# Kernel optimization log

Hardware: AMD Instinct MI355X
Metric: run time of the kernel (lower is better)

Reference implementation:

```python
import jax, jax.numpy as jnp
import numpy as np

B, T, C, H = 4, 2048, 2048, 16
HD = C // H  # head_size = 128
EPS = 1e-5


def layernorm(x, g, b):
    mu = jnp.mean(x, axis=-1, keepdims=True)
    var = jnp.var(x, axis=-1, keepdims=True)
    return (x - mu) * jax.lax.rsqrt(var + EPS) * g + b


def setup_inputs() -> dict:
    key = jax.random.key(0)
    ks = jax.random.split(key, 12)
    s_attn = 1.0 / np.sqrt(C)
    s_ffn1 = 1.0 / np.sqrt(C)
    s_ffn2 = 1.0 / np.sqrt(4 * C)
    return {
        "x": jax.random.normal(ks[0], (B, T, C), jnp.float32),
        "Wq": jax.random.normal(ks[1], (H, C, HD), jnp.float32) * s_attn,
        "Wk": jax.random.normal(ks[2], (H, C, HD), jnp.float32) * s_attn,
        "Wv": jax.random.normal(ks[3], (H, C, HD), jnp.float32) * s_attn,
        "Wp": jax.random.normal(ks[4], (C, C), jnp.float32) * s_attn,
        "bp": jnp.zeros((C,), jnp.float32),
        "W1": jax.random.normal(ks[5], (C, 4 * C), jnp.float32) * s_ffn1,
        "b1": jnp.zeros((4 * C,), jnp.float32),
        "W2": jax.random.normal(ks[6], (4 * C, C), jnp.float32) * s_ffn2,
        "b2": jnp.zeros((C,), jnp.float32),
        "g1": jnp.ones((C,), jnp.float32),
        "beta1": jnp.zeros((C,), jnp.float32),
        "g2": jnp.ones((C,), jnp.float32),
        "beta2": jnp.zeros((C,), jnp.float32),
    }


def reference(x, Wq, Wk, Wv, Wp, bp, W1, b1, W2, b2, g1, beta1, g2, beta2):
    # --- attention sublayer (pre-LN, causal) ---
    h = layernorm(x, g1, beta1)
    q = jnp.einsum("btc,hcd->bhtd", h, Wq)
    k = jnp.einsum("bsc,hcd->bhsd", h, Wk)
    v = jnp.einsum("bsc,hcd->bhsd", h, Wv)
    scores = jnp.einsum("bhtd,bhsd->bhts", q, k) / jnp.sqrt(jnp.asarray(HD, x.dtype))
    causal = jnp.tril(jnp.ones((T, T), bool))
    scores = jnp.where(causal, scores, jnp.asarray(-jnp.inf, x.dtype))
    w = jax.nn.softmax(scores, axis=-1)  # dropout = identity (eval mode)
    o = jnp.einsum("bhts,bhsd->bhtd", w, v)
    o = o.transpose(0, 2, 1, 3).reshape(B, T, C)  # concat heads
    x = x + o @ Wp + bp
    # --- feed-forward sublayer ---
    h2 = layernorm(x, g2, beta2)
    f = jax.nn.gelu(h2 @ W1 + b1, approximate=False)
    x = x + f @ W2 + b2
    return x
```

## Files before the change

### kernel.cpp

```cpp
#include <hip/hip_runtime.h>
#include <math.h>

#define B_ 4
#define T_ 2048
#define C_ 2048
#define H_ 16
#define HD_ 128

typedef __attribute__((ext_vector_type(8))) short short8;
typedef __attribute__((ext_vector_type(4))) float f32x4;
typedef unsigned short u16;
typedef unsigned int u32;

__device__ __forceinline__ u16 f2bf(float f) {
  union { float f; unsigned u; } v; v.f = f;
  unsigned r = v.u + 0x7FFFu + ((v.u >> 16) & 1u);
  return (u16)(r >> 16);
}

__device__ __forceinline__ void gld16(const void* g, void* l) {
  __builtin_amdgcn_global_load_lds(
      (__attribute__((address_space(1))) void*)(void*)g,
      (__attribute__((address_space(3))) void*)l, 16, 0, 0);
}

__global__ __launch_bounds__(256) void tconv(const float* __restrict__ in,
                                             u16* __restrict__ out,
                                             int K, int N,
                                             long inBS, long outBS) {
  __shared__ float tile[32][33];
  const float* inb = in + (long)blockIdx.z * inBS;
  u16* outb = out + (long)blockIdx.z * outBS;
  int k0 = blockIdx.x << 5, n0 = blockIdx.y << 5;
  int t = threadIdx.x;
  {
    int kk = t >> 3, nn = (t & 7) << 2;
    float4 v = *(const float4*)(inb + (long)(k0 + kk) * N + n0 + nn);
    tile[kk][nn + 0] = v.x; tile[kk][nn + 1] = v.y;
    tile[kk][nn + 2] = v.z; tile[kk][nn + 3] = v.w;
  }
  __syncthreads();
  {
    int nn = t >> 3, kk = (t & 7) << 2;
    ushort4 o;
    o.x = f2bf(tile[kk + 0][nn]); o.y = f2bf(tile[kk + 1][nn]);
    o.z = f2bf(tile[kk + 2][nn]); o.w = f2bf(tile[kk + 3][nn]);
    *(ushort4*)(outb + (long)(n0 + nn) * K + k0 + kk) = o;
  }
}

__global__ __launch_bounds__(256) void ln_rows(const float* __restrict__ x,
                                               const float* __restrict__ gam,
                                               const float* __restrict__ bet,
                                               u16* __restrict__ out) {
  int row = blockIdx.x;
  const float* xr = x + (size_t)row * C_;
  int t = threadIdx.x;
  float4 v0 = *(const float4*)(xr + t * 8);
  float4 v1 = *(const float4*)(xr + t * 8 + 4);
  float s = v0.x + v0.y + v0.z + v0.w + v1.x + v1.y + v1.z + v1.w;
  float ss = v0.x * v0.x + v0.y * v0.y + v0.z * v0.z + v0.w * v0.w +
             v1.x * v1.x + v1.y * v1.y + v1.z * v1.z + v1.w * v1.w;
  for (int d = 32; d > 0; d >>= 1) {
    s += __shfl_down(s, d);
    ss += __shfl_down(ss, d);
  }
  __shared__ float red[8];
  int wv = t >> 6;
  if ((t & 63) == 0) { red[wv] = s; red[4 + wv] = ss; }
  __syncthreads();
  s = red[0] + red[1] + red[2] + red[3];
  ss = red[4] + red[5] + red[6] + red[7];
  float mu = s * (1.0f / C_);
  float var = ss * (1.0f / C_) - mu * mu;
  float rs = rsqrtf(var + 1e-5f);
  int c = t * 8;
  float vv[8] = {v0.x, v0.y, v0.z, v0.w, v1.x, v1.y, v1.z, v1.w};
  ushort4 o0, o1;
  o0.x = f2bf((vv[0] - mu) * rs * gam[c + 0] + bet[c + 0]);
  o0.y = f2bf((vv[1] - mu) * rs * gam[c + 1] + bet[c + 1]);
  o0.z = f2bf((vv[2] - mu) * rs * gam[c + 2] + bet[c + 2]);
  o0.w = f2bf((vv[3] - mu) * rs * gam[c + 3] + bet[c + 3]);
  o1.x = f2bf((vv[4] - mu) * rs * gam[c + 4] + bet[c + 4]);
  o1.y = f2bf((vv[5] - mu) * rs * gam[c + 5] + bet[c + 5]);
  o1.z = f2bf((vv[6] - mu) * rs * gam[c + 6] + bet[c + 6]);
  o1.w = f2bf((vv[7] - mu) * rs * gam[c + 7] + bet[c + 7]);
  *(ushort4*)(out + (size_t)row * C_ + c) = o0;
  *(ushort4*)(out + (size_t)row * C_ + c + 4) = o1;
}

template <int EPI>
__global__ __launch_bounds__(512, 2) void gemm256(
    const u16* __restrict__ A, const u16* __restrict__ BT,
    int M, int N, int K, int lda, int ldb,
    u16* __restrict__ oq, u16* __restrict__ ok, u16* __restrict__ ovt,
    float* __restrict__ of32, const float* __restrict__ resid,
    const float* __restrict__ bias, u16* __restrict__ obf, int addBias) {
  extern __shared__ char smem[];
  int nbx = N >> 8;
  int nwg = gridDim.x;
  int flat = blockIdx.x;
  int sw = (flat & 7) * (nwg >> 3) + (flat >> 3);
  int bx = sw % nbx, by = sw / nbx;
  int m0 = by << 8, n0 = bx << 8;
  int tid = threadIdx.x;
  int lane = tid & 63, wave = tid >> 6;
  int wm = wave >> 2, wn = wave & 3;
  int l15 = lane & 15, l16 = lane >> 4;
  int nt = K >> 6;

  f32x4 acc[8][4] = {};
  short8 afA[4][2], afB[4][2], bfA[2][2], bfB[2][2];

  auto stage = [&](int b, int r, int k0) {
    int row = (r & 3) * 64 + (tid >> 3);
    int lslot = (tid & 7) ^ (row & 7);
    char* dst = smem + ((r < 4) ? 0 : 65536) + b * 32768 + (r & 3) * 8192 + tid * 16;
    const u16* src = ((r < 4) ? (A + (long)(m0 + row) * lda)
                              : (BT + (long)(n0 + row) * ldb)) +
                     k0 + lslot * 8;
    gld16(src, dst);
  };
  auto ldA = [&](int cur, int mf, int kk) {
    int row = wm * 128 + mf * 16 + l15;
    int slot = (kk * 4 + l16) ^ (row & 7);
    return *(const short8*)(smem + cur * 32768 + row * 128 + slot * 16);
  };
  auto ldB = [&](int cur, int nf, int kk) {
    int row = wn * 64 + nf * 16 + l15;
    int slot = (kk * 4 + l16) ^ (row & 7);
    return *(const short8*)(smem + 65536 + cur * 32768 + row * 128 + slot * 16);
  };

#pragma unroll
  for (int r = 0; r < 8; ++r) stage(0, r, 0);
  __syncthreads();

#pragma unroll
  for (int mq = 0; mq < 4; ++mq)
#pragma unroll
    for (int kk = 0; kk < 2; ++kk) afA[mq][kk] = ldA(0, mq, kk);
#pragma unroll
  for (int nq = 0; nq < 2; ++nq)
#pragma unroll
    for (int kk = 0; kk < 2; ++kk) bfA[nq][kk] = ldB(0, nq, kk);

  for (int t = 0; t < nt; ++t) {
    int cur = t & 1, nxt = cur ^ 1;
    bool more = (t + 1) < nt;
    int k1 = (t + 1) << 6;
    if (more) {
#pragma unroll
      for (int r = 0; r < 8; ++r) stage(nxt, r, k1);
    }
#pragma unroll
    for (int nq = 0; nq < 2; ++nq)
#pragma unroll
      for (int kk = 0; kk < 2; ++kk) bfB[nq][kk] = ldB(cur, 2 + nq, kk);
    __builtin_amdgcn_s_setprio(1);
#pragma unroll
    for (int mq = 0; mq < 4; ++mq)
#pragma unroll
      for (int nq = 0; nq < 2; ++nq)
#pragma unroll
        for (int kk = 0; kk < 2; ++kk)
          acc[mq][nq] = __builtin_amdgcn_mfma_f32_16x16x32_bf16(
              afA[mq][kk], bfA[nq][kk], acc[mq][nq], 0, 0, 0);
    __builtin_amdgcn_s_setprio(0);
#pragma unroll
    for (int mq = 0; mq < 4; ++mq)
#pragma unroll
      for (int kk = 0; kk < 2; ++kk) afB[mq][kk] = ldA(cur, 4 + mq, kk);
    __builtin_amdgcn_s_setprio(1);
#pragma unroll
    for (int mq = 0; mq < 4; ++mq)
#pragma unroll
      for (int nq = 0; nq < 2; ++nq)
#pragma unroll
        for (int kk = 0; kk < 2; ++kk)
          acc[mq][2 + nq] = __builtin_amdgcn_mfma_f32_16x16x32_bf16(
              afA[mq][kk], bfB[nq][kk], acc[mq][2 + nq], 0, 0, 0);
    __builtin_amdgcn_s_setprio(0);
    __builtin_amdgcn_s_setprio(1);
#pragma unroll
    for (int mq = 0; mq < 4; ++mq)
#pragma unroll
      for (int nq = 0; nq < 2; ++nq)
#pragma unroll
        for (int kk = 0; kk < 2; ++kk)
          acc[4 + mq][nq] = __builtin_amdgcn_mfma_f32_16x16x32_bf16(
              afB[mq][kk], bfA[nq][kk], acc[4 + mq][nq], 0, 0, 0);
    __builtin_amdgcn_s_setprio(0);
    __builtin_amdgcn_s_setprio(1);
#pragma unroll
    for (int mq = 0; mq < 4; ++mq)
#pragma unroll
      for (int nq = 0; nq < 2; ++nq)
#pragma unroll
        for (int kk = 0; kk < 2; ++kk)
          acc[4 + mq][2 + nq] = __builtin_amdgcn_mfma_f32_16x16x32_bf16(
              afB[mq][kk], bfB[nq][kk], acc[4 + mq][2 + nq], 0, 0, 0);
    __builtin_amdgcn_s_setprio(0);
    if (more) {
      __syncthreads();
#pragma unroll
      for (int mq = 0; mq < 4; ++mq)
#pragma unroll
        for (int kk = 0; kk < 2; ++kk) afA[mq][kk] = ldA(nxt, mq, kk);
#pragma unroll
      for (int nq = 0; nq < 2; ++nq)
#pragma unroll
        for (int kk = 0; kk < 2; ++kk) bfA[nq][kk] = ldB(nxt, nq, kk);
    }
  }

#pragma unroll
  for (int mf = 0; mf < 8; ++mf) {
#pragma unroll
    for (int nf = 0; nf < 4; ++nf) {
      int rowf = m0 + wm * 128 + mf * 16 + l16 * 4;
      int col = n0 + wn * 64 + nf * 16 + l15;
      if constexpr (EPI == 0) {
        int seg = col >> 11, cn = col & 2047;
        int hh = cn >> 7, dd = cn & 127;
        int bb = rowf >> 11, t0 = rowf & 2047;
        if (seg == 2) {
          ushort4 o;
          o.x = f2bf(acc[mf][nf][0]); o.y = f2bf(acc[mf][nf][1]);
          o.z = f2bf(acc[mf][nf][2]); o.w = f2bf(acc[mf][nf][3]);
          *(ushort4*)(ovt + ((long)(bb * H_ + hh) * HD_ + dd) * T_ + t0) = o;
        } else {
          u16* dst = (seg == 0) ? oq : ok;
#pragma unroll
          for (int r = 0; r < 4; ++r)
            dst[((long)(bb * H_ + hh) * T_ + t0 + r) * HD_ + dd] =
                f2bf(acc[mf][nf][r]);
        }
      } else if constexpr (EPI == 1) {
#pragma unroll
        for (int r = 0; r < 4; ++r) {
          long idx = (long)(rowf + r) * N + col;
          of32[idx] = resid[idx] + bias[col] + acc[mf][nf][r];
        }
      } else if constexpr (EPI == 2) {
#pragma unroll
        for (int r = 0; r < 4; ++r) {
          float v = acc[mf][nf][r] + bias[col];
          float g = 0.5f * v * (1.0f + erff(v * 0.70710678118654752f));
          obf[(long)(rowf + r) * N + col] = f2bf(g);
        }
      } else {
#pragma unroll
        for (int r = 0; r < 4; ++r) {
          long idx = (long)(rowf + r) * N + col;
          float v = acc[mf][nf][r];
          if (addBias) v += bias[col];
          of32[idx] += v;
        }
      }
    }
  }
}

__global__ __launch_bounds__(256) void attn_fwd(const u16* __restrict__ q,
                                                const u16* __restrict__ k,
                                                const u16* __restrict__ vt,
                                                u16* __restrict__ o) {
  extern __shared__ char asmem[];
  int bid = blockIdx.x;
  int bh = bid & 63;
  int qb = 31 - (bid >> 6);
  int q0 = qb << 6;
  int tid = threadIdx.x, lane = tid & 63, wave = tid >> 6;
  int l15 = lane & 15, l16 = lane >> 4;
  int wq0 = q0 + wave * 16;
  const u16* kbase = k + (long)bh * T_ * HD_;
  const u16* vbase = vt + (long)bh * HD_ * T_;
  char* Psw = asmem + 65536 + wave * 2048;

  short8 qf[4];
#pragma unroll
  for (int kk = 0; kk < 4; ++kk)
    qf[kk] = *(const short8*)(q + ((long)bh * T_ + wq0 + l15) * HD_ +
                              kk * 32 + l16 * 8);

  f32x4 accO[8] = {};
  float m_r[4], l_r[4];
#pragma unroll
  for (int r = 0; r < 4; ++r) { m_r[r] = -INFINITY; l_r[r] = 0.f; }
  const float sc = 0.08838834764831845f * 1.4426950408889634f;

  int nt = qb + 1;

  auto stage = [&](int b, int t) {
    int s0 = t << 6;
    char* Kd = asmem + b * 16384;
    char* Vd = asmem + 32768 + b * 16384;
#pragma unroll
    for (int r = 0; r < 4; ++r) {
      int off = r * 4096 + tid * 16;
      int krow = off >> 8;
      int kslot = (tid & 15) ^ (krow & 7);
      gld16(kbase + (long)(s0 + krow) * HD_ + kslot * 8, Kd + off);
      int dd = off >> 7;
      int vslot = (tid & 7) ^ (dd & 7);
      gld16(vbase + (long)dd * T_ + s0 + vslot * 8, Vd + off);
    }
  };

  stage(0, 0);
  asm volatile("s_waitcnt vmcnt(0)" ::: "memory");
  __syncthreads();

  for (int t = 0; t < nt; ++t) {
    int s0 = t << 6;
    int cur = t & 1;
    bool more = (t + 1 < nt);
    if (more) stage(cur ^ 1, t + 1);

    if (s0 <= wq0 + 15) {
      const char* Kc = asmem + cur * 16384;
      const char* Vc = asmem + 32768 + cur * 16384;
      bool needmask = (s0 + 63 > wq0);
      f32x4 S[4];
#pragma unroll
      for (int sb = 0; sb < 4; ++sb) {
        f32x4 s = {};
#pragma unroll
        for (int kk = 0; kk < 4; ++kk) {
          int srow = sb * 16 + l15;
          int kb = srow * 256 + (((kk * 4 + l16) ^ (srow & 7)) << 4);
          short8 kf = *(const short8*)(Kc + kb);
          s = __builtin_amdgcn_mfma_f32_16x16x32_bf16(qf[kk], kf, s, 0, 0, 0);
        }
        S[sb] = s;
      }
      float mxl[4];
      bool growL = false;
#pragma unroll
      for (int r = 0; r < 4; ++r) {
        int tt = wq0 + 4 * l16 + r;
        float mx = -INFINITY;
#pragma unroll
        for (int sb = 0; sb < 4; ++sb) {
          float v = S[sb][r] * sc;
          if (needmask && (s0 + sb * 16 + l15 > tt)) v = -INFINITY;
          S[sb][r] = v;
          mx = fmaxf(mx, v);
        }
        mxl[r] = mx;
        growL = growL || (mx > m_r[r] + 8.0f);
      }
      bool anyg = __any(growL);
      float al[4];
      if (anyg) {
#pragma unroll
        for (int r = 0; r < 4; ++r) {
          float mx = mxl[r];
          mx = fmaxf(mx, __shfl_xor(mx, 1));
          mx = fmaxf(mx, __shfl_xor(mx, 2));
          mx = fmaxf(mx, __shfl_xor(mx, 4));
          mx = fmaxf(mx, __shfl_xor(mx, 8));
          float mo = m_r[r];
          float mn = fmaxf(mo, mx);
          al[r] = exp2f(mo - mn);
          m_r[r] = mn;
        }
      } else {
#pragma unroll
        for (int r = 0; r < 4; ++r) al[r] = 1.0f;
      }
#pragma unroll
      for (int r = 0; r < 4; ++r) {
        float mn = m_r[r];
        int prow = 4 * l16 + r;
        float rs = 0.f;
#pragma unroll
        for (int sb = 0; sb < 4; ++sb) {
          float p = exp2f(S[sb][r] - mn);
          rs += p;
          int pb = (prow * 128 + (sb * 16 + l15) * 2) ^ ((prow & 7) << 4);
          *(u16*)(Psw + pb) = f2bf(p);
        }
        rs += __shfl_xor(rs, 1);
        rs += __shfl_xor(rs, 2);
        rs += __shfl_xor(rs, 4);
        rs += __shfl_xor(rs, 8);
        l_r[r] = l_r[r] * al[r] + rs;
      }
      if (anyg) {
#pragma unroll
        for (int db = 0; db < 8; ++db)
#pragma unroll
          for (int r = 0; r < 4; ++r) accO[db][r] *= al[r];
      }
      short8 pf[2];
#pragma unroll
      for (int st = 0; st < 2; ++st) {
        int prow = l15;
        int pb = (prow * 128 + (st * 4 + l16) * 16) ^ ((prow & 7) << 4);
        pf[st] = *(const short8*)(Psw + pb);
      }
#pragma unroll
      for (int db = 0; db < 8; ++db) {
#pragma unroll
        for (int st = 0; st < 2; ++st) {
          int vrow = db * 16 + l15;
          int vb = (vrow * 128 + (st * 4 + l16) * 16) ^ ((vrow & 7) << 4);
          short8 vf = *(const short8*)(Vc + vb);
          accO[db] = __builtin_amdgcn_mfma_f32_16x16x32_bf16(pf[st], vf,
                                                             accO[db], 0, 0, 0);
        }
      }
    }
    if (more) asm volatile("s_waitcnt vmcnt(0)" ::: "memory");
    __syncthreads();
  }

  int bb = bh >> 4, hh = bh & 15;
  float inv[4];
#pragma unroll
  for (int r = 0; r < 4; ++r) inv[r] = 1.0f / l_r[r];
#pragma unroll
  for (int db = 0; db < 8; ++db)
#pragma unroll
    for (int r = 0; r < 4; ++r) {
      int tt = wq0 + 4 * l16 + r;
      o[((long)bb * T_ + tt) * C_ + hh * HD_ + db * 16 + l15] =
          f2bf(accO[db][r] * inv[r]);
    }
}

extern "C" void kernel_launch(void* const* d_in, const int* in_sizes, int n_in,
                              void* d_out, int out_size, void* d_ws, size_t ws_size,
                              hipStream_t stream) {
  (void)in_sizes; (void)n_in; (void)out_size; (void)ws_size;
  const float* x   = (const float*)d_in[0];
  const float* Wq  = (const float*)d_in[1];
  const float* Wk  = (const float*)d_in[2];
  const float* Wv  = (const float*)d_in[3];
  const float* Wp  = (const float*)d_in[4];
  const float* bp  = (const float*)d_in[5];
  const float* W1  = (const float*)d_in[6];
  const float* b1  = (const float*)d_in[7];
  const float* W2  = (const float*)d_in[8];
  const float* b2  = (const float*)d_in[9];
  const float* g1  = (const float*)d_in[10];
  const float* be1 = (const float*)d_in[11];
  const float* g2  = (const float*)d_in[12];
  const float* be2 = (const float*)d_in[13];
  float* out = (float*)d_out;

  (void)hipFuncSetAttribute((const void*)gemm256<0>,
                            hipFuncAttributeMaxDynamicSharedMemorySize, 131072);
  (void)hipFuncSetAttribute((const void*)gemm256<1>,
                            hipFuncAttributeMaxDynamicSharedMemorySize, 131072);
  (void)hipFuncSetAttribute((const void*)gemm256<2>,
                            hipFuncAttributeMaxDynamicSharedMemorySize, 131072);
  (void)hipFuncSetAttribute((const void*)gemm256<3>,
                            hipFuncAttributeMaxDynamicSharedMemorySize, 131072);
  (void)hipFuncSetAttribute((const void*)attn_fwd,
                            hipFuncAttributeMaxDynamicSharedMemorySize, 73728);

  char* ws = (char*)d_ws;
  size_t off = 0;
  auto alloc = [&](size_t n) {
    void* p = ws + off;
    off += (n + 255) & ~(size_t)255;
    return p;
  };
  u16* wqkvT = (u16*)alloc((size_t)6144 * 2048 * 2);
  u16* wpT   = (u16*)alloc((size_t)2048 * 2048 * 2);
  u16* w1T   = (u16*)alloc((size_t)8192 * 2048 * 2);
  u16* w2T   = (u16*)alloc((size_t)2048 * 8192 * 2);
  u16* hb    = (u16*)alloc((size_t)8192 * 2048 * 2);
  u16* qbuf  = (u16*)alloc((size_t)8192 * 2048 * 2);
  u16* kbuf  = (u16*)alloc((size_t)8192 * 2048 * 2);
  u16* vtbuf = (u16*)alloc((size_t)8192 * 2048 * 2);
  u16* ob = hb;
  u16* fb = qbuf;

  tconv<<<dim3(64, 4, 16), 256, 0, stream>>>(Wq, wqkvT, 2048, 128,
                                             (long)2048 * 128, (long)128 * 2048);
  tconv<<<dim3(64, 4, 16), 256, 0, stream>>>(Wk, wqkvT + (size_t)2048 * 2048, 2048, 128,
                                             (long)2048 * 128, (long)128 * 2048);
  tconv<<<dim3(64, 4, 16), 256, 0, stream>>>(Wv, wqkvT + (size_t)4096 * 2048, 2048, 128,
                                             (long)2048 * 128, (long)128 * 2048);
  tconv<<<dim3(64, 64, 1), 256, 0, stream>>>(Wp, wpT, 2048, 2048, 0, 0);
  tconv<<<dim3(64, 256, 1), 256, 0, stream>>>(W1, w1T, 2048, 8192, 0, 0);
  tconv<<<dim3(256, 64, 1), 256, 0, stream>>>(W2, w2T, 8192, 2048, 0, 0);

  ln_rows<<<8192, 256, 0, stream>>>(x, g1, be1, hb);
  gemm256<0><<<768, 512, 131072, stream>>>(hb, wqkvT, 8192, 6144, 2048, 2048, 2048,
                                           qbuf, kbuf, vtbuf, nullptr, nullptr,
                                           nullptr, nullptr, 0);
  attn_fwd<<<2048, 256, 73728, stream>>>(qbuf, kbuf, vtbuf, ob);
  gemm256<1><<<256, 512, 131072, stream>>>(ob, wpT, 8192, 2048, 2048, 2048, 2048,
                                           nullptr, nullptr, nullptr, out, x, bp,
                                           nullptr, 0);

  ln_rows<<<8192, 256, 0, stream>>>(out, g2, be2, hb);
  for (int c = 0; c < 2; ++c) {
    gemm256<2><<<512, 512, 131072, stream>>>(hb, w1T + (size_t)c * 4096 * 2048,
                                             8192, 4096, 2048, 2048, 2048,
                                             nullptr, nullptr, nullptr, nullptr,
                                             nullptr, b1 + c * 4096, fb, 0);
    gemm256<3><<<256, 512, 131072, stream>>>(fb, w2T + (size_t)c * 4096,
                                             8192, 2048, 4096, 4096, 8192,
                                             nullptr, nullptr, nullptr, out,
                                             nullptr, b2, nullptr, c == 0 ? 1 : 0);
  }
}
```

Baseline: 1.113 ms.

## Shrink attention KV tile to 32, fold softmax scale into Q, truncate P to bf16

```diff
diff --git a/kernel.cpp b/kernel.cpp
--- a/kernel.cpp
+++ b/kernel.cpp
@@ -16,6 +16,11 @@
   union { float f; unsigned u; } v; v.f = f;
   unsigned r = v.u + 0x7FFFu + ((v.u >> 16) & 1u);
   return (u16)(r >> 16);
+}
+
+__device__ __forceinline__ u16 f2bf_trunc(float f) {
+  union { float f; unsigned u; } v; v.f = f;
+  return (u16)(v.u >> 16);
 }
 
 __device__ __forceinline__ void gld16(const void* g, void* l) {
@@ -229,11 +234,16 @@
           o.x = f2bf(acc[mf][nf][0]); o.y = f2bf(acc[mf][nf][1]);
           o.z = f2bf(acc[mf][nf][2]); o.w = f2bf(acc[mf][nf][3]);
           *(ushort4*)(ovt + ((long)(bb * H_ + hh) * HD_ + dd) * T_ + t0) = o;
+        } else if (seg == 0) {
+          const float qs = 0.08838834764831845f * 1.4426950408889634f;
+#pragma unroll
+          for (int r = 0; r < 4; ++r)
+            oq[((long)(bb * H_ + hh) * T_ + t0 + r) * HD_ + dd] =
+                f2bf(acc[mf][nf][r] * qs);
         } else {
-          u16* dst = (seg == 0) ? oq : ok;
 #pragma unroll
           for (int r = 0; r < 4; ++r)
-            dst[((long)(bb * H_ + hh) * T_ + t0 + r) * HD_ + dd] =
+            ok[((long)(bb * H_ + hh) * T_ + t0 + r) * HD_ + dd] =
                 f2bf(acc[mf][nf][r]);
         }
       } else if constexpr (EPI == 1) {
@@ -276,7 +286,7 @@
   int wq0 = q0 + wave * 16;
   const u16* kbase = k + (long)bh * T_ * HD_;
   const u16* vbase = vt + (long)bh * HD_ * T_;
-  char* Psw = asmem + 65536 + wave * 2048;
+  char* Psw = asmem + 32768 + wave * 1024;
 
   short8 qf[4];
 #pragma unroll
@@ -288,22 +298,21 @@
   float m_r[4], l_r[4];
 #pragma unroll
   for (int r = 0; r < 4; ++r) { m_r[r] = -INFINITY; l_r[r] = 0.f; }
-  const float sc = 0.08838834764831845f * 1.4426950408889634f;
-
-  int nt = qb + 1;
+
+  int nt = 2 * qb + 2;
 
   auto stage = [&](int b, int t) {
-    int s0 = t << 6;
-    char* Kd = asmem + b * 16384;
-    char* Vd = asmem + 32768 + b * 16384;
-#pragma unroll
-    for (int r = 0; r < 4; ++r) {
+    int s0 = t << 5;
+    char* Kd = asmem + b * 8192;
+    char* Vd = asmem + 16384 + b * 8192;
+#pragma unroll
+    for (int r = 0; r < 2; ++r) {
       int off = r * 4096 + tid * 16;
       int krow = off >> 8;
       int kslot = (tid & 15) ^ (krow & 7);
       gld16(kbase + (long)(s0 + krow) * HD_ + kslot * 8, Kd + off);
-      int dd = off >> 7;
-      int vslot = (tid & 7) ^ (dd & 7);
+      int dd = off >> 6;
+      int vslot = (tid & 3) ^ (dd & 3);
       gld16(vbase + (long)dd * T_ + s0 + vslot * 8, Vd + off);
     }
   };
@@ -313,18 +322,18 @@
   __syncthreads();
 
   for (int t = 0; t < nt; ++t) {
-    int s0 = t << 6;
+    int s0 = t << 5;
     int cur = t & 1;
     bool more = (t + 1 < nt);
     if (more) stage(cur ^ 1, t + 1);
 
     if (s0 <= wq0 + 15) {
-      const char* Kc = asmem + cur * 16384;
-      const char* Vc = asmem + 32768 + cur * 16384;
-      bool needmask = (s0 + 63 > wq0);
-      f32x4 S[4];
-#pragma unroll
-      for (int sb = 0; sb < 4; ++sb) {
+      const char* Kc = asmem + cur * 8192;
+      const char* Vc = asmem + 16384 + cur * 8192;
+      bool needmask = (s0 + 31 > wq0);
+      f32x4 S[2];
+#pragma unroll
+      for (int sb = 0; sb < 2; ++sb) {
         f32x4 s = {};
 #pragma unroll
         for (int kk = 0; kk < 4; ++kk) {
@@ -342,8 +351,8 @@
         int tt = wq0 + 4 * l16 + r;
         float mx = -INFINITY;
 #pragma unroll
-        for (int sb = 0; sb < 4; ++sb) {
-          float v = S[sb][r] * sc;
+        for (int sb = 0; sb < 2; ++sb) {
+          float v = S[sb][r];
           if (needmask && (s0 + sb * 16 + l15 > tt)) v = -INFINITY;
           S[sb][r] = v;
           mx = fmaxf(mx, v);
@@ -376,11 +385,13 @@
         int prow = 4 * l16 + r;
         float rs = 0.f;
 #pragma unroll
-        for (int sb = 0; sb < 4; ++sb) {
+        for (int sb = 0; sb < 2; ++sb) {
           float p = exp2f(S[sb][r] - mn);
           rs += p;
-          int pb = (prow * 128 + (sb * 16 + l15) * 2) ^ ((prow & 7) << 4);
-          *(u16*)(Psw + pb) = f2bf(p);
+          int col = sb * 16 + l15;
+          int slot = col >> 3;
+          int pb = prow * 64 + ((slot ^ l16) << 4) + (col & 7) * 2;
+          *(u16*)(Psw + pb) = f2bf_trunc(p);
         }
         rs += __shfl_xor(rs, 1);
         rs += __shfl_xor(rs, 2);
@@ -394,23 +405,15 @@
 #pragma unroll
           for (int r = 0; r < 4; ++r) accO[db][r] *= al[r];
       }
-      short8 pf[2];
-#pragma unroll
-      for (int st = 0; st < 2; ++st) {
-        int prow = l15;
-        int pb = (prow * 128 + (st * 4 + l16) * 16) ^ ((prow & 7) << 4);
-        pf[st] = *(const short8*)(Psw + pb);
-      }
+      int pslot = l16 ^ ((l15 >> 2) & 3);
+      short8 pf = *(const short8*)(Psw + l15 * 64 + (pslot << 4));
 #pragma unroll
       for (int db = 0; db < 8; ++db) {
-#pragma unroll
-        for (int st = 0; st < 2; ++st) {
-          int vrow = db * 16 + l15;
-          int vb = (vrow * 128 + (st * 4 + l16) * 16) ^ ((vrow & 7) << 4);
-          short8 vf = *(const short8*)(Vc + vb);
-          accO[db] = __builtin_amdgcn_mfma_f32_16x16x32_bf16(pf[st], vf,
-                                                             accO[db], 0, 0, 0);
-        }
+        int vrow = db * 16 + l15;
+        int vb = vrow * 64 + ((l16 ^ (vrow & 3)) << 4);
+        short8 vf = *(const short8*)(Vc + vb);
+        accO[db] = __builtin_amdgcn_mfma_f32_16x16x32_bf16(pf, vf,
+                                                           accO[db], 0, 0, 0);
       }
     }
     if (more) asm volatile("s_waitcnt vmcnt(0)" ::: "memory");
@@ -460,7 +463,7 @@
   (void)hipFuncSetAttribute((const void*)gemm256<3>,
                             hipFuncAttributeMaxDynamicSharedMemorySize, 131072);
   (void)hipFuncSetAttribute((const void*)attn_fwd,
-                            hipFuncAttributeMaxDynamicSharedMemorySize, 73728);
+                            hipFuncAttributeMaxDynamicSharedMemorySize, 36864);
 
   char* ws = (char*)d_ws;
   size_t off = 0;
@@ -494,7 +497,7 @@
   gemm256<0><<<768, 512, 131072, stream>>>(hb, wqkvT, 8192, 6144, 2048, 2048, 2048,
                                            qbuf, kbuf, vtbuf, nullptr, nullptr,
                                            nullptr, nullptr, 0);
-  attn_fwd<<<2048, 256, 73728, stream>>>(qbuf, kbuf, vtbuf, ob);
+  attn_fwd<<<2048, 256, 36864, stream>>>(qbuf, kbuf, vtbuf, ob);
   gemm256<1><<<256, 512, 131072, stream>>>(ob, wpT, 8192, 2048, 2048, 2048, 2048,
                                            nullptr, nullptr, nullptr, out, x, bp,
                                            nullptr, 0);
```

New measurement: 1.117 ms. About the same (+0.4%).
